# Kernel optimization log

Measured on AMD Instinct MI355X. Metric: run time of the kernel, lower is better.

The kernel has to match this reference:

```python
import jax, jax.numpy as jnp
import numpy as np

N = 50000      # num_nodes
R = 51         # num relations (after enrichment: inverse + self-loop)
E = 16         # emb_dim
C = 8          # num_classes
B = 40         # bases
NNZ = 1_600_000  # number of triples / nonzeros per adjacency


def setup_inputs() -> dict:
    key = jax.random.key(0)
    ks = jax.random.split(key, 7)
    # random triples (s, p, o)
    s = jax.random.randint(ks[0], (NNZ,), 0, N, dtype=jnp.int32)
    o = jax.random.randint(ks[1], (NNZ,), 0, N, dtype=jnp.int32)
    p = jax.random.randint(ks[2], (NNZ,), 0, R, dtype=jnp.int32)
    # horizontal adjacency: A_hor[s, p*N + o];  vertical: A_ver[p*N + s, o]
    hor_rows = s
    hor_cols = p * N + o
    ver_rows = p * N + s
    ver_cols = o
    # values = ones / row-sum of vertical graph (sum_sparse_rgcn normalization),
    # shared by hor and ver graphs as in the torch module
    deg = jax.ops.segment_sum(jnp.ones((NNZ,), jnp.float32), ver_rows,
                              num_segments=R * N)
    values = 1.0 / deg[ver_rows]
    # parameters (basis decomposition for both layers)
    comps1 = jax.random.normal(ks[3], (R, B), dtype=jnp.float32) * 0.05
    bases1 = jax.random.normal(ks[4], (B, N, E), dtype=jnp.float32) * 0.05
    comps2 = jax.random.normal(ks[5], (R, B), dtype=jnp.float32) * 0.05
    bases2 = jax.random.normal(ks[6], (B, E, C), dtype=jnp.float32) * 0.05
    bias1 = jnp.zeros((E,), jnp.float32)
    bias2 = jnp.zeros((C,), jnp.float32)
    return {
        'values': values, 'comps1': comps1, 'bases1': bases1,
        'comps2': comps2, 'bases2': bases2, 'bias1': bias1, 'bias2': bias2,
        'hor_rows': hor_rows, 'hor_cols': hor_cols,
        'ver_rows': ver_rows, 'ver_cols': ver_cols,
    }


def reference(values, comps1, bases1, comps2, bases2, bias1, bias2,
              hor_rows, hor_cols, ver_rows, ver_cols):
    b, n, e = bases1.shape
    r = comps1.shape[0]
    c = bases2.shape[2]
    # layer 1: basis-composed weights (r, n, e) -> flat (r*n, e)
    W1 = jnp.matmul(comps1, bases1.reshape(b, n * e)).reshape(r * n, e)
    # h = hor_graph @ W1   (sparse (n, r*n) x dense (r*n, e)) via gather+scatter
    h = jax.ops.segment_sum(values[:, None] * W1[hor_cols], hor_rows,
                            num_segments=n)          # (n, e)
    h = jax.nn.relu(h + bias1)
    # hv = ver_graph @ h   (sparse (r*n, n) x dense (n, e))
    hv = jax.ops.segment_sum(values[:, None] * h[ver_cols], ver_rows,
                             num_segments=r * n).reshape(r, n, e)
    # layer 2: basis-composed weights (r, e, c), bmm + sum over relations
    W2 = jnp.matmul(comps2, bases2.reshape(b, e * c)).reshape(r, e, c)
    out = jnp.einsum('rne,rec->nc', hv, W2) + bias2   # (n, c)
    return out
```

## Files before the change

kernel.cpp:

```cpp
#include <hip/hip_runtime.h>
#include <hip/hip_bf16.h>

constexpr int N   = 50000;
constexpr int R   = 51;
constexpr int E   = 16;
constexpr int C   = 8;
constexpr int B   = 40;
constexpr int NNZ = 1600000;

constexpr int BSH  = 6;
constexpr int BKN  = 1 << BSH;
constexpr int NB   = (N + BKN - 1) >> BSH;
constexpr int NPAD = NB * BKN;
constexpr int KS   = 2;

constexpr int CBLK   = 784;
constexpr int CCHUNK = (NNZ + CBLK - 1) / CBLK;
constexpr int SBLK   = 256;
constexpr int SCHUNK = (NNZ + SBLK - 1) / SBLK;

__global__ __launch_bounds__(256) void w1_gemm_kernel(
    const float* __restrict__ comps1, const float* __restrict__ bases1,
    unsigned* __restrict__ W1u) {
  constexpr int NC2 = N * E / 2;
  int j = blockIdx.x * 256 + threadIdx.x;
  if (j >= NC2) return;
  const float2* b2 = reinterpret_cast<const float2*>(bases1);
  float2 col[B];
#pragma unroll
  for (int b = 0; b < B; ++b) col[b] = b2[b * NC2 + j];
#pragma unroll 1
  for (int r = 0; r < R; ++r) {
    float ax = 0.f, ay = 0.f;
#pragma unroll
    for (int b = 0; b < B; ++b) {
      float cc = comps1[r * B + b];
      ax = fmaf(cc, col[b].x, ax);
      ay = fmaf(cc, col[b].y, ay);
    }
    unsigned lo = __bfloat16_as_ushort(__float2bfloat16(ax));
    unsigned hi = __bfloat16_as_ushort(__float2bfloat16(ay));
    W1u[r * NC2 + j] = (hi << 16) | lo;
  }
}

__global__ __launch_bounds__(256) void count_kernel(
    const int* __restrict__ rows, int* __restrict__ gcount) {
  __shared__ int hist[NB];
  for (int i = threadIdx.x; i < NB; i += 256) hist[i] = 0;
  __syncthreads();
  int lo = blockIdx.x * CCHUNK;
  int hi = lo + CCHUNK < NNZ ? lo + CCHUNK : NNZ;
  for (int i = lo + threadIdx.x; i < hi; i += 256)
    atomicAdd(&hist[rows[i] >> BSH], 1);
  __syncthreads();
  for (int i = threadIdx.x; i < NB; i += 256)
    if (hist[i]) atomicAdd(&gcount[i], hist[i]);
}

__global__ __launch_bounds__(1024) void scan_kernel(
    const int* __restrict__ gcount, int* __restrict__ gstart,
    int* __restrict__ gcursor) {
  __shared__ int buf[1024];
  int t = threadIdx.x;
  int own = (t < NB) ? gcount[t] : 0;
  buf[t] = own;
  __syncthreads();
  for (int d = 1; d < 1024; d <<= 1) {
    int v = (t >= d) ? buf[t - d] : 0;
    __syncthreads();
    buf[t] += v;
    __syncthreads();
  }
  if (t < NB) {
    int st = buf[t] - own;
    gstart[t] = st;
    gcursor[t] = st;
  }
  if (t == NB - 1) gstart[NB] = buf[t];
}

__global__ __launch_bounds__(256) void scatter_kernel(
    const int* __restrict__ rows, const int* __restrict__ cols,
    const float* __restrict__ vals, int* __restrict__ gcursor,
    int2* __restrict__ packed) {
  __shared__ int hist[NB];
  __shared__ int base[NB];
  for (int i = threadIdx.x; i < NB; i += 256) hist[i] = 0;
  __syncthreads();
  int lo = blockIdx.x * SCHUNK;
  int hi = lo + SCHUNK < NNZ ? lo + SCHUNK : NNZ;
  for (int i = lo + threadIdx.x; i < hi; i += 256)
    atomicAdd(&hist[rows[i] >> BSH], 1);
  __syncthreads();
  for (int i = threadIdx.x; i < NB; i += 256) {
    int c = hist[i];
    base[i] = c ? atomicAdd(&gcursor[i], c) : 0;
  }
  __syncthreads();
  for (int i = threadIdx.x; i < NB; i += 256) hist[i] = 0;
  __syncthreads();
  for (int i = lo + threadIdx.x; i < hi; i += 256) {
    int s = rows[i];
    int b = s >> BSH;
    int pos = base[b] + atomicAdd(&hist[b], 1);
    packed[pos] = make_int2(((s & (BKN - 1)) << 26) | cols[i],
                            __float_as_int(vals[i]));
  }
}

__global__ void w2_gemm_kernel(const float* __restrict__ comps2,
                               const float* __restrict__ bases2,
                               float* __restrict__ W2g) {
  int i = blockIdx.x * blockDim.x + threadIdx.x;
  if (i >= R * E * C) return;
  int r = i >> 7;
  int ec = i & 127;
  float acc = 0.f;
#pragma unroll
  for (int b = 0; b < B; ++b)
    acc = fmaf(comps2[r * B + b], bases2[b * 128 + ec], acc);
  W2g[i] = acc;
}

__device__ __forceinline__ void l1_accum(float* hp, float v, uint4 w0, uint4 w1) {
  atomicAdd(hp + 0,  v * __uint_as_float(w0.x << 16));
  atomicAdd(hp + 1,  v * __uint_as_float(w0.x & 0xffff0000u));
  atomicAdd(hp + 2,  v * __uint_as_float(w0.y << 16));
  atomicAdd(hp + 3,  v * __uint_as_float(w0.y & 0xffff0000u));
  atomicAdd(hp + 4,  v * __uint_as_float(w0.z << 16));
  atomicAdd(hp + 5,  v * __uint_as_float(w0.z & 0xffff0000u));
  atomicAdd(hp + 6,  v * __uint_as_float(w0.w << 16));
  atomicAdd(hp + 7,  v * __uint_as_float(w0.w & 0xffff0000u));
  atomicAdd(hp + 8,  v * __uint_as_float(w1.x << 16));
  atomicAdd(hp + 9,  v * __uint_as_float(w1.x & 0xffff0000u));
  atomicAdd(hp + 10, v * __uint_as_float(w1.y << 16));
  atomicAdd(hp + 11, v * __uint_as_float(w1.y & 0xffff0000u));
  atomicAdd(hp + 12, v * __uint_as_float(w1.z << 16));
  atomicAdd(hp + 13, v * __uint_as_float(w1.z & 0xffff0000u));
  atomicAdd(hp + 14, v * __uint_as_float(w1.w << 16));
  atomicAdd(hp + 15, v * __uint_as_float(w1.w & 0xffff0000u));
}

__global__ __launch_bounds__(256) void layer1_kernel(
    const unsigned* __restrict__ W1u, const int* __restrict__ gstart,
    const int2* __restrict__ packed, float* __restrict__ hpart) {
  __shared__ float hacc[BKN * 17];
  for (int i = threadIdx.x; i < BKN * 17; i += 256) hacc[i] = 0.f;
  __syncthreads();
  int bkt = blockIdx.x >> 1, part = blockIdx.x & 1;
  int lo = gstart[bkt], len = gstart[bkt + 1] - lo;
  int a = lo + ((len * part) >> 1), b = lo + ((len * (part + 1)) >> 1);
  const uint4* W14 = reinterpret_cast<const uint4*>(W1u);
  const long long* pk8 = reinterpret_cast<const long long*>(packed);
  int e = a + (int)threadIdx.x;
  while (e + 768 < b) {
    long long r0 = __builtin_nontemporal_load(pk8 + e);
    long long r1 = __builtin_nontemporal_load(pk8 + e + 256);
    long long r2 = __builtin_nontemporal_load(pk8 + e + 512);
    long long r3 = __builtin_nontemporal_load(pk8 + e + 768);
    int m0 = (int)r0, m1 = (int)r1, m2 = (int)r2, m3 = (int)r3;
    int c0 = m0 & ((1 << 26) - 1), c1 = m1 & ((1 << 26) - 1);
    int c2 = m2 & ((1 << 26) - 1), c3 = m3 & ((1 << 26) - 1);
    uint4 wa0 = W14[c0 * 2 + 0], wa1 = W14[c0 * 2 + 1];
    uint4 wb0 = W14[c1 * 2 + 0], wb1 = W14[c1 * 2 + 1];
    uint4 wc0 = W14[c2 * 2 + 0], wc1 = W14[c2 * 2 + 1];
    uint4 wd0 = W14[c3 * 2 + 0], wd1 = W14[c3 * 2 + 1];
    l1_accum(&hacc[(((unsigned)m0) >> 26) * 17], __int_as_float((int)(r0 >> 32)), wa0, wa1);
    l1_accum(&hacc[(((unsigned)m1) >> 26) * 17], __int_as_float((int)(r1 >> 32)), wb0, wb1);
    l1_accum(&hacc[(((unsigned)m2) >> 26) * 17], __int_as_float((int)(r2 >> 32)), wc0, wc1);
    l1_accum(&hacc[(((unsigned)m3) >> 26) * 17], __int_as_float((int)(r3 >> 32)), wd0, wd1);
    e += 1024;
  }
  while (e < b) {
    long long r0 = __builtin_nontemporal_load(pk8 + e);
    int m0 = (int)r0;
    int c0 = m0 & ((1 << 26) - 1);
    uint4 w0 = W14[c0 * 2 + 0], w1 = W14[c0 * 2 + 1];
    l1_accum(&hacc[(((unsigned)m0) >> 26) * 17], __int_as_float((int)(r0 >> 32)), w0, w1);
    e += 256;
  }
  __syncthreads();
  float* dst = hpart + (size_t)part * (NPAD * E) + ((size_t)bkt << BSH) * E;
  for (int i = threadIdx.x; i < BKN * E; i += 256) {
    int slo = i >> 4, ee = i & 15;
    dst[i] = hacc[slo * 17 + ee];
  }
}

__global__ __launch_bounds__(256) void relu_kernel(
    const float* __restrict__ hpart, const float* __restrict__ bias1,
    float* __restrict__ h) {
  int i = blockIdx.x * 256 + threadIdx.x;
  if (i >= N * E / 4) return;
  constexpr int P4 = NPAD * E / 4;
  const float4* hp = reinterpret_cast<const float4*>(hpart);
  float4 s0 = hp[i], s1 = hp[i + P4];
  float4 bb = reinterpret_cast<const float4*>(bias1)[i & 3];
  float4 r;
  r.x = fmaxf(s0.x + s1.x + bb.x, 0.f);
  r.y = fmaxf(s0.y + s1.y + bb.y, 0.f);
  r.z = fmaxf(s0.z + s1.z + bb.z, 0.f);
  r.w = fmaxf(s0.w + s1.w + bb.w, 0.f);
  reinterpret_cast<float4*>(h)[i] = r;
}

__device__ __forceinline__ void l2_accum(float* op, float v, float4 h0,
                                         float4 h1, float4 h2, float4 h3,
                                         const float* w2s, int p) {
  const float4* wp = reinterpret_cast<const float4*>(w2s + p * 132);
#pragma unroll
  for (int c = 0; c < 8; ++c) {
    float4 aq = wp[c * 4 + 0];
    float4 bq = wp[c * 4 + 1];
    float4 cq = wp[c * 4 + 2];
    float4 dq = wp[c * 4 + 3];
    float s = h0.x * aq.x + h0.y * aq.y + h0.z * aq.z + h0.w * aq.w
            + h1.x * bq.x + h1.y * bq.y + h1.z * bq.z + h1.w * bq.w
            + h2.x * cq.x + h2.y * cq.y + h2.z * cq.z + h2.w * cq.w
            + h3.x * dq.x + h3.y * dq.y + h3.z * dq.z + h3.w * dq.w;
    atomicAdd(op + c, v * s);
  }
}

__global__ __launch_bounds__(256) void layer2_kernel(
    const float* __restrict__ h, const float* __restrict__ W2g,
    const int* __restrict__ gstart, const int2* __restrict__ packed,
    float* __restrict__ opart) {
  __shared__ float w2s[R * 132];
  __shared__ float oacc[BKN * 9];
  for (int i = threadIdx.x; i < R * E * C; i += 256) {
    int p = i >> 7, ec = i & 127;
    int e = ec >> 3, c = ec & 7;
    w2s[p * 132 + c * 16 + e] = W2g[i];
  }
  for (int i = threadIdx.x; i < BKN * 9; i += 256) oacc[i] = 0.f;
  __syncthreads();
  int bkt = blockIdx.x >> 1, part = blockIdx.x & 1;
  int lo = gstart[bkt], len = gstart[bkt + 1] - lo;
  int a = lo + ((len * part) >> 1), b = lo + ((len * (part + 1)) >> 1);
  const float4* H4 = reinterpret_cast<const float4*>(h);
  const long long* pk8 = reinterpret_cast<const long long*>(packed);
  int e = a + (int)threadIdx.x;
  while (e + 256 < b) {
    long long r0 = __builtin_nontemporal_load(pk8 + e);
    long long r1 = __builtin_nontemporal_load(pk8 + e + 256);
    int m0 = (int)r0, m1 = (int)r1;
    int col0 = m0 & ((1 << 26) - 1), col1 = m1 & ((1 << 26) - 1);
    int p0 = (int)((unsigned)col0 / (unsigned)N);
    int o0 = col0 - p0 * N;
    int p1 = (int)((unsigned)col1 / (unsigned)N);
    int o1 = col1 - p1 * N;
    float4 a0 = H4[o0 * 4 + 0], a1 = H4[o0 * 4 + 1];
    float4 a2 = H4[o0 * 4 + 2], a3 = H4[o0 * 4 + 3];
    float4 b0 = H4[o1 * 4 + 0], b1 = H4[o1 * 4 + 1];
    float4 b2 = H4[o1 * 4 + 2], b3 = H4[o1 * 4 + 3];
    l2_accum(&oacc[(((unsigned)m0) >> 26) * 9], __int_as_float((int)(r0 >> 32)),
             a0, a1, a2, a3, w2s, p0);
    l2_accum(&oacc[(((unsigned)m1) >> 26) * 9], __int_as_float((int)(r1 >> 32)),
             b0, b1, b2, b3, w2s, p1);
    e += 512;
  }
  while (e < b) {
    long long r0 = __builtin_nontemporal_load(pk8 + e);
    int m0 = (int)r0;
    int col0 = m0 & ((1 << 26) - 1);
    int p0 = (int)((unsigned)col0 / (unsigned)N);
    int o0 = col0 - p0 * N;
    float4 a0 = H4[o0 * 4 + 0], a1 = H4[o0 * 4 + 1];
    float4 a2 = H4[o0 * 4 + 2], a3 = H4[o0 * 4 + 3];
    l2_accum(&oacc[(((unsigned)m0) >> 26) * 9], __int_as_float((int)(r0 >> 32)),
             a0, a1, a2, a3, w2s, p0);
    e += 256;
  }
  __syncthreads();
  float* dst = opart + (size_t)part * (NPAD * C) + ((size_t)bkt << BSH) * C;
  for (int i = threadIdx.x; i < BKN * C; i += 256) {
    int slo = i >> 3, c = i & 7;
    dst[i] = oacc[slo * 9 + c];
  }
}

__global__ __launch_bounds__(256) void out_kernel(
    const float* __restrict__ opart, const float* __restrict__ bias2,
    float* __restrict__ out) {
  int i = blockIdx.x * 256 + threadIdx.x;
  if (i >= N * C / 4) return;
  constexpr int P4 = NPAD * C / 4;
  const float4* op = reinterpret_cast<const float4*>(opart);
  float4 s0 = op[i], s1 = op[i + P4];
  float4 bb = reinterpret_cast<const float4*>(bias2)[i & 1];
  float4 r;
  r.x = s0.x + s1.x + bb.x;
  r.y = s0.y + s1.y + bb.y;
  r.z = s0.z + s1.z + bb.z;
  r.w = s0.w + s1.w + bb.w;
  reinterpret_cast<float4*>(out)[i] = r;
}

extern "C" void kernel_launch(void* const* d_in, const int* in_sizes, int n_in,
                              void* d_out, int out_size, void* d_ws, size_t ws_size,
                              hipStream_t stream) {
  const float* values  = (const float*)d_in[0];
  const float* comps1  = (const float*)d_in[1];
  const float* bases1  = (const float*)d_in[2];
  const float* comps2  = (const float*)d_in[3];
  const float* bases2  = (const float*)d_in[4];
  const float* bias1   = (const float*)d_in[5];
  const float* bias2   = (const float*)d_in[6];
  const int* hor_rows  = (const int*)d_in[7];
  const int* hor_cols  = (const int*)d_in[8];
  float* out = (float*)d_out;

  char* ws = (char*)d_ws;
  size_t off = 0;
  auto alloc = [&](size_t bytes) {
    void* p = ws + off;
    off += (bytes + 255) & ~size_t(255);
    return p;
  };
  unsigned* W1u    = (unsigned*)alloc((size_t)R * N * E / 2 * 4);
  float*    h      = (float*)alloc((size_t)N * E * 4);
  float*    W2g    = (float*)alloc((size_t)R * E * C * 4);
  int*      gcount = (int*)alloc((size_t)NB * 4);
  int*      gstart = (int*)alloc((size_t)(NB + 1) * 4);
  int*      gcursor= (int*)alloc((size_t)NB * 4);
  int2*     packed = (int2*)alloc((size_t)NNZ * 8);
  float*    hpart  = (float*)alloc((size_t)KS * NPAD * E * 4);
  float*    opart  = (float*)alloc((size_t)KS * NPAD * C * 4);
  (void)ws_size; (void)in_sizes; (void)n_in; (void)out_size;

  hipMemsetAsync(gcount, 0, (size_t)NB * 4, stream);

  count_kernel<<<CBLK, 256, 0, stream>>>(hor_rows, gcount);
  scan_kernel<<<1, 1024, 0, stream>>>(gcount, gstart, gcursor);
  scatter_kernel<<<SBLK, 256, 0, stream>>>(hor_rows, hor_cols, values, gcursor,
                                           packed);
  w2_gemm_kernel<<<(R * E * C + 255) / 256, 256, 0, stream>>>(comps2, bases2, W2g);
  w1_gemm_kernel<<<(N * E / 2 + 255) / 256, 256, 0, stream>>>(comps1, bases1, W1u);
  layer1_kernel<<<NB * KS, 256, 0, stream>>>(W1u, gstart, packed, hpart);
  relu_kernel<<<(N * E / 4 + 255) / 256, 256, 0, stream>>>(hpart, bias1, h);
  layer2_kernel<<<NB * KS, 256, 0, stream>>>(h, W2g, gstart, packed, opart);
  out_kernel<<<(N * C / 4 + 255) / 256, 256, 0, stream>>>(opart, bias2, out);
}
```

Before: 585.8 us.

## Sort buckets by relation, split work four ways, and launch kernels in halves

A new pass sorts each row bucket's packed entries by relation index so that consecutive gathers hit nearby rows of W1. Each bucket is now split across four blocks instead of two, with matching four-way reductions in the relu and output kernels. Threads now process adjacent entry pairs rather than strided ones. The W1 GEMM and both layer kernels are launched as two halves. The sort adds an extra read and write of the packed array and is skipped for buckets above a capacity limit, and the split launches add launch overhead with no clear benefit.

Result: slower. 625.7 us (+6.8%).

```diff
diff --git a/kernel.cpp b/kernel.cpp
--- a/kernel.cpp
+++ b/kernel.cpp
@@ -11,20 +11,23 @@
 constexpr int BSH  = 6;
 constexpr int BKN  = 1 << BSH;
 constexpr int NB   = (N + BKN - 1) >> BSH;
+constexpr int NB2  = NB / 2;
 constexpr int NPAD = NB * BKN;
-constexpr int KS   = 2;
+constexpr int KS   = 4;
 
 constexpr int CBLK   = 784;
 constexpr int CCHUNK = (NNZ + CBLK - 1) / CBLK;
 constexpr int SBLK   = 256;
 constexpr int SCHUNK = (NNZ + SBLK - 1) / SBLK;
+constexpr int PSCAP  = 2816;
+constexpr int CMASK  = (1 << 26) - 1;
 
 __global__ __launch_bounds__(256) void w1_gemm_kernel(
     const float* __restrict__ comps1, const float* __restrict__ bases1,
-    unsigned* __restrict__ W1u) {
+    unsigned* __restrict__ W1u, int jbase, int jend) {
   constexpr int NC2 = N * E / 2;
-  int j = blockIdx.x * 256 + threadIdx.x;
-  if (j >= NC2) return;
+  int j = jbase + blockIdx.x * 256 + threadIdx.x;
+  if (j >= jend) return;
   const float2* b2 = reinterpret_cast<const float2*>(bases1);
   float2 col[B];
 #pragma unroll
@@ -106,6 +109,38 @@
     int pos = base[b] + atomicAdd(&hist[b], 1);
     packed[pos] = make_int2(((s & (BKN - 1)) << 26) | cols[i],
                             __float_as_int(vals[i]));
+  }
+}
+
+__global__ __launch_bounds__(256) void psort_kernel(
+    const int* __restrict__ gstart, long long* __restrict__ packed) {
+  __shared__ long long buf[PSCAP];
+  __shared__ int cnt[R + 1];
+  __shared__ int base[R + 1];
+  int bkt = blockIdx.x;
+  int lo = gstart[bkt], len = gstart[bkt + 1] - lo;
+  if (len > PSCAP) return;
+  if (threadIdx.x < R + 1) cnt[threadIdx.x] = 0;
+  __syncthreads();
+  for (int i = threadIdx.x; i < len; i += 256) {
+    long long r = packed[lo + i];
+    buf[i] = r;
+    int p = (int)((unsigned)((int)r & CMASK) / (unsigned)N);
+    atomicAdd(&cnt[p], 1);
+  }
+  __syncthreads();
+  if (threadIdx.x == 0) {
+    int run = 0;
+    for (int p = 0; p < R; ++p) { base[p] = run; run += cnt[p]; }
+  }
+  __syncthreads();
+  if (threadIdx.x < R + 1) cnt[threadIdx.x] = 0;
+  __syncthreads();
+  for (int i = threadIdx.x; i < len; i += 256) {
+    long long r = buf[i];
+    int p = (int)((unsigned)((int)r & CMASK) / (unsigned)N);
+    int pos = base[p] + atomicAdd(&cnt[p], 1);
+    packed[lo + pos] = r;
   }
 }
 
@@ -144,41 +179,33 @@
 
 __global__ __launch_bounds__(256) void layer1_kernel(
     const unsigned* __restrict__ W1u, const int* __restrict__ gstart,
-    const int2* __restrict__ packed, float* __restrict__ hpart) {
+    const int2* __restrict__ packed, float* __restrict__ hpart, int bkt_base) {
   __shared__ float hacc[BKN * 17];
   for (int i = threadIdx.x; i < BKN * 17; i += 256) hacc[i] = 0.f;
   __syncthreads();
-  int bkt = blockIdx.x >> 1, part = blockIdx.x & 1;
+  int bkt = bkt_base + (blockIdx.x >> 2), part = blockIdx.x & 3;
   int lo = gstart[bkt], len = gstart[bkt + 1] - lo;
-  int a = lo + ((len * part) >> 1), b = lo + ((len * (part + 1)) >> 1);
+  int a = lo + ((len * part) >> 2), b = lo + ((len * (part + 1)) >> 2);
+  int plen = b - a;
   const uint4* W14 = reinterpret_cast<const uint4*>(W1u);
   const long long* pk8 = reinterpret_cast<const long long*>(packed);
-  int e = a + (int)threadIdx.x;
-  while (e + 768 < b) {
+  for (int e = a + 2 * (int)threadIdx.x; e + 1 < b; e += 512) {
     long long r0 = __builtin_nontemporal_load(pk8 + e);
-    long long r1 = __builtin_nontemporal_load(pk8 + e + 256);
-    long long r2 = __builtin_nontemporal_load(pk8 + e + 512);
-    long long r3 = __builtin_nontemporal_load(pk8 + e + 768);
-    int m0 = (int)r0, m1 = (int)r1, m2 = (int)r2, m3 = (int)r3;
-    int c0 = m0 & ((1 << 26) - 1), c1 = m1 & ((1 << 26) - 1);
-    int c2 = m2 & ((1 << 26) - 1), c3 = m3 & ((1 << 26) - 1);
+    long long r1 = __builtin_nontemporal_load(pk8 + e + 1);
+    int m0 = (int)r0, m1 = (int)r1;
+    int c0 = m0 & CMASK, c1 = m1 & CMASK;
     uint4 wa0 = W14[c0 * 2 + 0], wa1 = W14[c0 * 2 + 1];
     uint4 wb0 = W14[c1 * 2 + 0], wb1 = W14[c1 * 2 + 1];
-    uint4 wc0 = W14[c2 * 2 + 0], wc1 = W14[c2 * 2 + 1];
-    uint4 wd0 = W14[c3 * 2 + 0], wd1 = W14[c3 * 2 + 1];
     l1_accum(&hacc[(((unsigned)m0) >> 26) * 17], __int_as_float((int)(r0 >> 32)), wa0, wa1);
     l1_accum(&hacc[(((unsigned)m1) >> 26) * 17], __int_as_float((int)(r1 >> 32)), wb0, wb1);
-    l1_accum(&hacc[(((unsigned)m2) >> 26) * 17], __int_as_float((int)(r2 >> 32)), wc0, wc1);
-    l1_accum(&hacc[(((unsigned)m3) >> 26) * 17], __int_as_float((int)(r3 >> 32)), wd0, wd1);
-    e += 1024;
-  }
-  while (e < b) {
+  }
+  int m = a + ((plen >> 1) << 1);
+  for (int e = m + (int)threadIdx.x; e < b; e += 256) {
     long long r0 = __builtin_nontemporal_load(pk8 + e);
     int m0 = (int)r0;
-    int c0 = m0 & ((1 << 26) - 1);
+    int c0 = m0 & CMASK;
     uint4 w0 = W14[c0 * 2 + 0], w1 = W14[c0 * 2 + 1];
     l1_accum(&hacc[(((unsigned)m0) >> 26) * 17], __int_as_float((int)(r0 >> 32)), w0, w1);
-    e += 256;
   }
   __syncthreads();
   float* dst = hpart + (size_t)part * (NPAD * E) + ((size_t)bkt << BSH) * E;
@@ -195,13 +222,13 @@
   if (i >= N * E / 4) return;
   constexpr int P4 = NPAD * E / 4;
   const float4* hp = reinterpret_cast<const float4*>(hpart);
-  float4 s0 = hp[i], s1 = hp[i + P4];
+  float4 s0 = hp[i], s1 = hp[i + P4], s2 = hp[i + 2 * P4], s3 = hp[i + 3 * P4];
   float4 bb = reinterpret_cast<const float4*>(bias1)[i & 3];
   float4 r;
-  r.x = fmaxf(s0.x + s1.x + bb.x, 0.f);
-  r.y = fmaxf(s0.y + s1.y + bb.y, 0.f);
-  r.z = fmaxf(s0.z + s1.z + bb.z, 0.f);
-  r.w = fmaxf(s0.w + s1.w + bb.w, 0.f);
+  r.x = fmaxf(s0.x + s1.x + s2.x + s3.x + bb.x, 0.f);
+  r.y = fmaxf(s0.y + s1.y + s2.y + s3.y + bb.y, 0.f);
+  r.z = fmaxf(s0.z + s1.z + s2.z + s3.z + bb.z, 0.f);
+  r.w = fmaxf(s0.w + s1.w + s2.w + s3.w + bb.w, 0.f);
   reinterpret_cast<float4*>(h)[i] = r;
 }
 
@@ -226,7 +253,7 @@
 __global__ __launch_bounds__(256) void layer2_kernel(
     const float* __restrict__ h, const float* __restrict__ W2g,
     const int* __restrict__ gstart, const int2* __restrict__ packed,
-    float* __restrict__ opart) {
+    float* __restrict__ opart, int bkt_base) {
   __shared__ float w2s[R * 132];
   __shared__ float oacc[BKN * 9];
   for (int i = threadIdx.x; i < R * E * C; i += 256) {
@@ -236,17 +263,17 @@
   }
   for (int i = threadIdx.x; i < BKN * 9; i += 256) oacc[i] = 0.f;
   __syncthreads();
-  int bkt = blockIdx.x >> 1, part = blockIdx.x & 1;
+  int bkt = bkt_base + (blockIdx.x >> 2), part = blockIdx.x & 3;
   int lo = gstart[bkt], len = gstart[bkt + 1] - lo;
-  int a = lo + ((len * part) >> 1), b = lo + ((len * (part + 1)) >> 1);
+  int a = lo + ((len * part) >> 2), b = lo + ((len * (part + 1)) >> 2);
+  int plen = b - a;
   const float4* H4 = reinterpret_cast<const float4*>(h);
   const long long* pk8 = reinterpret_cast<const long long*>(packed);
-  int e = a + (int)threadIdx.x;
-  while (e + 256 < b) {
+  for (int e = a + 2 * (int)threadIdx.x; e + 1 < b; e += 512) {
     long long r0 = __builtin_nontemporal_load(pk8 + e);
-    long long r1 = __builtin_nontemporal_load(pk8 + e + 256);
+    long long r1 = __builtin_nontemporal_load(pk8 + e + 1);
     int m0 = (int)r0, m1 = (int)r1;
-    int col0 = m0 & ((1 << 26) - 1), col1 = m1 & ((1 << 26) - 1);
+    int col0 = m0 & CMASK, col1 = m1 & CMASK;
     int p0 = (int)((unsigned)col0 / (unsigned)N);
     int o0 = col0 - p0 * N;
     int p1 = (int)((unsigned)col1 / (unsigned)N);
@@ -259,19 +286,18 @@
              a0, a1, a2, a3, w2s, p0);
     l2_accum(&oacc[(((unsigned)m1) >> 26) * 9], __int_as_float((int)(r1 >> 32)),
              b0, b1, b2, b3, w2s, p1);
-    e += 512;
-  }
-  while (e < b) {
+  }
+  int m = a + ((plen >> 1) << 1);
+  for (int e = m + (int)threadIdx.x; e < b; e += 256) {
     long long r0 = __builtin_nontemporal_load(pk8 + e);
     int m0 = (int)r0;
-    int col0 = m0 & ((1 << 26) - 1);
+    int col0 = m0 & CMASK;
     int p0 = (int)((unsigned)col0 / (unsigned)N);
     int o0 = col0 - p0 * N;
     float4 a0 = H4[o0 * 4 + 0], a1 = H4[o0 * 4 + 1];
     float4 a2 = H4[o0 * 4 + 2], a3 = H4[o0 * 4 + 3];
     l2_accum(&oacc[(((unsigned)m0) >> 26) * 9], __int_as_float((int)(r0 >> 32)),
              a0, a1, a2, a3, w2s, p0);
-    e += 256;
   }
   __syncthreads();
   float* dst = opart + (size_t)part * (NPAD * C) + ((size_t)bkt << BSH) * C;
@@ -288,13 +314,13 @@
   if (i >= N * C / 4) return;
   constexpr int P4 = NPAD * C / 4;
   const float4* op = reinterpret_cast<const float4*>(opart);
-  float4 s0 = op[i], s1 = op[i + P4];
+  float4 s0 = op[i], s1 = op[i + P4], s2 = op[i + 2 * P4], s3 = op[i + 3 * P4];
   float4 bb = reinterpret_cast<const float4*>(bias2)[i & 1];
   float4 r;
-  r.x = s0.x + s1.x + bb.x;
-  r.y = s0.y + s1.y + bb.y;
-  r.z = s0.z + s1.z + bb.z;
-  r.w = s0.w + s1.w + bb.w;
+  r.x = s0.x + s1.x + s2.x + s3.x + bb.x;
+  r.y = s0.y + s1.y + s2.y + s3.y + bb.y;
+  r.z = s0.z + s1.z + s2.z + s3.z + bb.z;
+  r.w = s0.w + s1.w + s2.w + s3.w + bb.w;
   reinterpret_cast<float4*>(out)[i] = r;
 }
 
@@ -336,10 +362,14 @@
   scan_kernel<<<1, 1024, 0, stream>>>(gcount, gstart, gcursor);
   scatter_kernel<<<SBLK, 256, 0, stream>>>(hor_rows, hor_cols, values, gcursor,
                                            packed);
+  psort_kernel<<<NB, 256, 0, stream>>>(gstart, (long long*)packed);
   w2_gemm_kernel<<<(R * E * C + 255) / 256, 256, 0, stream>>>(comps2, bases2, W2g);
-  w1_gemm_kernel<<<(N * E / 2 + 255) / 256, 256, 0, stream>>>(comps1, bases1, W1u);
-  layer1_kernel<<<NB * KS, 256, 0, stream>>>(W1u, gstart, packed, hpart);
+  w1_gemm_kernel<<<782, 256, 0, stream>>>(comps1, bases1, W1u, 0, 200000);
+  w1_gemm_kernel<<<782, 256, 0, stream>>>(comps1, bases1, W1u, 200000, 400000);
+  layer1_kernel<<<NB2 * KS, 256, 0, stream>>>(W1u, gstart, packed, hpart, 0);
+  layer1_kernel<<<(NB - NB2) * KS, 256, 0, stream>>>(W1u, gstart, packed, hpart, NB2);
   relu_kernel<<<(N * E / 4 + 255) / 256, 256, 0, stream>>>(hpart, bias1, h);
-  layer2_kernel<<<NB * KS, 256, 0, stream>>>(h, W2g, gstart, packed, opart);
+  layer2_kernel<<<NB2 * KS, 256, 0, stream>>>(h, W2g, gstart, packed, opart, 0);
+  layer2_kernel<<<(NB - NB2) * KS, 256, 0, stream>>>(h, W2g, gstart, packed, opart, NB2);
   out_kernel<<<(N * C / 4 + 255) / 256, 256, 0, stream>>>(opart, bias2, out);
 }
```
